# Kernel tuning notes

Hardware: AMD Instinct MI355X
Metric: run time of the kernel (lower is better)

Reference implementation:

```python
import jax, jax.numpy as jnp
import numpy as np

DIM = 256


def setup_inputs() -> dict:
    key = jax.random.key(0)
    ks = jax.random.split(key, 10)
    d = DIM
    inp = {
        "agent": jax.random.normal(ks[0], (64, d), dtype=jnp.float32),
        "x": jax.random.normal(ks[1], (8, 4096, d), dtype=jnp.float32),
        # parameters (stored as [in, out]; y = x @ W + b)
        "W_qkv": jax.random.normal(ks[2], (d, 3 * d), dtype=jnp.float32) * (d ** -0.5),
        "b_qkv": jnp.zeros((3 * d,), dtype=jnp.float32),
        "W_agent": jax.random.normal(ks[3], (d, 2 * d), dtype=jnp.float32) * (d ** -0.5),
        "b_agent": jnp.zeros((2 * d,), dtype=jnp.float32),
        "W_fc1": jax.random.normal(ks[4], (d, d), dtype=jnp.float32) * (d ** -0.5),
        "b_fc1": jnp.zeros((d,), dtype=jnp.float32),
        "W_fc2": jax.random.normal(ks[5], (d, d), dtype=jnp.float32) * (d ** -0.5),
        "b_fc2": jnp.zeros((d,), dtype=jnp.float32),
    }
    return inp


def reference(agent, x, W_qkv, b_qkv, W_agent, b_agent, W_fc1, b_fc1, W_fc2, b_fc2):
    d = x.shape[-1]
    scale = d ** -0.5
    # qkv projection of tokens: [B,N,3d] -> q,k,v each [B,N,d]
    qkv = x @ W_qkv + b_qkv
    q, k, v = jnp.split(qkv, 3, axis=-1)
    # agent projection: [K,2d] -> q_agent,k_agent each [K,d]
    ag = agent @ W_agent + b_agent
    q_agent, k_agent = jnp.split(ag, 2, axis=-1)
    # stage 1: agents attend over tokens -> [B,K,N]
    attn1 = jax.nn.softmax(jnp.einsum('kd,bnd->bkn', q_agent, k) * scale, axis=-1)
    va = jnp.einsum('bkn,bnd->bkd', attn1, v)  # [B,K,d]
    va = va @ W_fc1 + b_fc1
    # stage 2: tokens attend over agents -> [B,N,K]
    attn2 = jax.nn.softmax(jnp.einsum('bnd,kd->bnk', q, k_agent) * scale, axis=-1)
    out = jnp.einsum('bnk,bkd->bnd', attn2, va)  # [B,N,d]
    out = out @ W_fc2 + b_fc2
    return out + x
```

## Files before the change

kernel.cpp:

```cpp
#include <hip/hip_runtime.h>
#include <stdint.h>
#include <string.h>

#define BB 8
#define NN 4096
#define DD 256
#define SCALE 0.0625f
#define XS 264
#define XT 72

using frag_ab = __attribute__((ext_vector_type(8))) short;
using frag_cd = __attribute__((ext_vector_type(4))) float;

__device__ __forceinline__ unsigned short f2bf(float f) {
    union { float f; unsigned u; } a; a.f = f;
    unsigned r = a.u + 0x7FFFu + ((a.u >> 16) & 1u);
    return (unsigned short)(r >> 16);
}
__device__ __forceinline__ float bf2f(unsigned short h) {
    union { unsigned u; float f; } a; a.u = ((unsigned)h) << 16;
    return a.f;
}
__device__ __forceinline__ int xsw(int tok, int d) {
    const int e = ((tok >> 3) & 3) << 1;
    return tok * XS + (d & 7) + (((d >> 3) ^ e) << 3);
}

__global__ __launch_bounds__(256) void k_setup(
    const float* __restrict__ agent, const float* __restrict__ Wag,
    const float* __restrict__ bag, const float* __restrict__ Wqkv,
    const float* __restrict__ bqkv, const float* __restrict__ Wfc1,
    const float* __restrict__ bfc1, const float* __restrict__ Wfc2,
    unsigned short* __restrict__ P12t, float* __restrict__ c2,
    unsigned short* __restrict__ W3b, float* __restrict__ b3)
{
    __shared__ float arow[256];
    __shared__ float red[4][256];
    float* redf = &red[0][0];
    const int bx = blockIdx.x, tid = threadIdx.x;
    const int w = tid >> 6, lane = tid & 63;
    if (bx < 128) {
        const int c = bx;
        const int woff = (c < 64) ? 256 : 0;
        const int aoff = (c < 64) ? 0 : 256;
        const int row = c & 63;
        {
            float p4[4] = {0.f, 0.f, 0.f, 0.f};
            for (int oo = 0; oo < 64; ++oo) {
                const int o = w * 64 + oo;
                const float ao = agent[row * 256 + o];
#pragma unroll
                for (int jj = 0; jj < 4; ++jj)
                    p4[jj] += ao * Wag[o * 512 + aoff + jj * 64 + lane];
            }
#pragma unroll
            for (int jj = 0; jj < 4; ++jj) red[w][jj * 64 + lane] = p4[jj];
        }
        __syncthreads();
        arow[tid] = bag[aoff + tid] + red[0][tid] + red[1][tid] + red[2][tid] + red[3][tid];
        __syncthreads();
        {
            const float4* wr = (const float4*)&Wqkv[(size_t)tid * 768 + woff];
            float s = 0.f;
#pragma unroll 4
            for (int o4 = 0; o4 < 64; ++o4) {
                float4 v = wr[o4];
                s += v.x * arow[o4 * 4] + v.y * arow[o4 * 4 + 1] +
                     v.z * arow[o4 * 4 + 2] + v.w * arow[o4 * 4 + 3];
            }
            P12t[(size_t)c * 256 + tid] = f2bf(SCALE * s);
        }
        if (c >= 64) {
            __syncthreads();
            redf[tid] = bqkv[woff + tid] * arow[tid];
            __syncthreads();
            for (int st = 128; st; st >>= 1) {
                if (tid < st) redf[tid] += redf[tid + st];
                __syncthreads();
            }
            if (tid == 0) c2[c - 64] = SCALE * redf[0];
        }
    } else {
        const int i = bx - 128;
        const bool isb3 = (bx == 384);
        {
            float p4[4] = {0.f, 0.f, 0.f, 0.f};
            for (int oo = 0; oo < 64; ++oo) {
                const int o = w * 64 + oo;
                const float wv = isb3 ? bqkv[512 + o] : Wqkv[(size_t)i * 768 + 512 + o];
#pragma unroll
                for (int jj = 0; jj < 4; ++jj)
                    p4[jj] += wv * Wfc1[o * 256 + jj * 64 + lane];
            }
#pragma unroll
            for (int jj = 0; jj < 4; ++jj) red[w][jj * 64 + lane] = p4[jj];
        }
        __syncthreads();
        arow[tid] = (isb3 ? bfc1[tid] : 0.f) +
                    red[0][tid] + red[1][tid] + red[2][tid] + red[3][tid];
        __syncthreads();
        {
            float p4[4] = {0.f, 0.f, 0.f, 0.f};
            for (int kk = 0; kk < 64; ++kk) {
                const int k = w * 64 + kk;
                const float av = arow[k];
#pragma unroll
                for (int jj = 0; jj < 4; ++jj)
                    p4[jj] += av * Wfc2[k * 256 + jj * 64 + lane];
            }
#pragma unroll
            for (int jj = 0; jj < 4; ++jj) red[w][jj * 64 + lane] = p4[jj];
        }
        __syncthreads();
        const float o4 = red[0][tid] + red[1][tid] + red[2][tid] + red[3][tid];
        if (isb3) b3[tid] = o4;
        else      W3b[(size_t)i * 256 + tid] = f2bf(o4);
    }
}

__global__ __launch_bounds__(256) void k_fuse(
    const float* __restrict__ x, const unsigned short* __restrict__ P12t,
    const float* __restrict__ c2, unsigned short* __restrict__ p2b,
    unsigned short* __restrict__ part, float* __restrict__ statS)
{
    __shared__ unsigned short xtile[64 * XS];
    __shared__ unsigned short Pl[64 * XT];
    __shared__ float Ss[4][64];
    const int s = blockIdx.x, b = blockIdx.y;
    const int n0 = s * 64;
    const int tid = threadIdx.x;
    const int w = tid >> 6, lane = tid & 63;
    const int ml = lane & 15, q = lane >> 4;

#pragma unroll
    for (int p = 0; p < 16; ++p) {
        int idx = p * 256 + tid;
        int tok = idx >> 6, d = (idx & 63) * 4;
        float4 v = *(const float4*)&x[(size_t)(b * 4096 + n0 + tok) * 256 + d];
        unsigned short u[4] = {f2bf(v.x), f2bf(v.y), f2bf(v.z), f2bf(v.w)};
        uint2 pk; memcpy(&pk, u, 8);
        *(uint2*)&xtile[xsw(tok, d)] = pk;
    }
    __syncthreads();

    frag_ab afr[8];
#pragma unroll
    for (int kb4 = 0; kb4 < 4; ++kb4)
#pragma unroll
        for (int ks = 0; ks < 2; ++ks)
            afr[kb4 * 2 + ks] =
                *(const frag_ab*)&xtile[xsw(w * 16 + ml, kb4 * 64 + ks * 32 + q * 8)];

    frag_cd acc1[8];
#pragma unroll
    for (int j = 0; j < 8; ++j)
#pragma unroll
        for (int r = 0; r < 4; ++r) acc1[j][r] = 0.f;

    for (int kb4 = 0; kb4 < 4; ++kb4) {
#pragma unroll
        for (int ks = 0; ks < 2; ++ks) {
            const int kk = kb4 * 64 + ks * 32 + q * 8;
            const frag_ab a = afr[kb4 * 2 + ks];
#pragma unroll
            for (int j = 0; j < 8; ++j) {
                frag_ab bf = *(const frag_ab*)&P12t[(size_t)(j * 16 + ml) * 256 + kk];
                acc1[j] = __builtin_amdgcn_mfma_f32_16x16x32_bf16(a, bf, acc1[j], 0, 0, 0);
            }
        }
    }

    {
        float cc[4];
#pragma unroll
        for (int j = 0; j < 4; ++j) cc[j] = c2[j * 16 + ml];
#pragma unroll
        for (int r = 0; r < 4; ++r) {
            float e[4], sum = 0.f;
#pragma unroll
            for (int j = 0; j < 4; ++j) {
                e[j] = __expf(acc1[4 + j][r] + cc[j]);
                sum += e[j];
            }
#pragma unroll
            for (int mask = 1; mask <= 8; mask <<= 1) sum += __shfl_xor(sum, mask);
            float inv = 1.f / sum;
            const int tok = n0 + w * 16 + q * 4 + r;
#pragma unroll
            for (int j = 0; j < 4; ++j)
                p2b[(size_t)(b * 4096 + tok) * 64 + j * 16 + ml] = f2bf(e[j] * inv);
        }
    }

    float e1[4][4];
#pragma unroll
    for (int j = 0; j < 4; ++j) {
#pragma unroll
        for (int r = 0; r < 4; ++r) e1[j][r] = __expf(acc1[j][r]);
        float sj = e1[j][0] + e1[j][1] + e1[j][2] + e1[j][3];
        sj += __shfl_xor(sj, 16);
        sj += __shfl_xor(sj, 32);
        if (lane < 16) Ss[w][j * 16 + ml] = sj;
    }

#pragma unroll
    for (int j = 0; j < 4; ++j)
#pragma unroll
        for (int r = 0; r < 4; ++r)
            Pl[(j * 16 + ml) * XT + w * 16 + q * 4 + r] = f2bf(e1[j][r]);
    __syncthreads();

    if (tid < 64)
        statS[(size_t)(b * 64 + tid) * 64 + s] =
            Ss[0][tid] + Ss[1][tid] + Ss[2][tid] + Ss[3][tid];

    frag_cd acc2[4][4];
#pragma unroll
    for (int af = 0; af < 4; ++af)
#pragma unroll
        for (int i = 0; i < 4; ++i)
#pragma unroll
            for (int r = 0; r < 4; ++r) acc2[af][i][r] = 0.f;
#pragma unroll
    for (int ks = 0; ks < 2; ++ks) {
        const int kk = ks * 32 + q * 8;
        frag_ab a[4], bf[4];
#pragma unroll
        for (int af = 0; af < 4; ++af)
            a[af] = *(const frag_ab*)&Pl[(af * 16 + ml) * XT + kk];
#pragma unroll
        for (int i = 0; i < 4; ++i) {
            const int d = w * 64 + i * 16 + ml;
            unsigned short u[8];
#pragma unroll
            for (int t = 0; t < 8; ++t) u[t] = xtile[xsw(kk + t, d)];
            memcpy(&bf[i], u, 16);
        }
#pragma unroll
        for (int af = 0; af < 4; ++af)
#pragma unroll
            for (int i = 0; i < 4; ++i)
                acc2[af][i] = __builtin_amdgcn_mfma_f32_16x16x32_bf16(
                    a[af], bf[i], acc2[af][i], 0, 0, 0);
    }
#pragma unroll
    for (int af = 0; af < 4; ++af)
#pragma unroll
        for (int i = 0; i < 4; ++i)
#pragma unroll
            for (int r = 0; r < 4; ++r)
                part[(size_t)((s * 8 + b) * 64 + af * 16 + q * 4 + r) * 256 +
                     w * 64 + i * 16 + ml] = f2bf(acc2[af][i][r]);
}

__global__ __launch_bounds__(256) void k_fc(
    const unsigned short* __restrict__ part, const float* __restrict__ statS,
    const unsigned short* __restrict__ W3b, const float* __restrict__ b3,
    unsigned short* __restrict__ va3t)
{
    __shared__ float red[4][256];
    __shared__ float rowb[256];
    __shared__ float rs[64];
    const int row = blockIdx.x, tid = threadIdx.x;
    const int b = row >> 6, agc = row & 63;
    const int w = tid >> 6, lane = tid & 63;
    {
        float p4[4] = {0.f, 0.f, 0.f, 0.f};
        for (int ss = 0; ss < 16; ++ss) {
            const int s = w * 16 + ss;
            uint2 pk = *(const uint2*)&part[(size_t)((s * 8 + b) * 64 + agc) * 256 + lane * 4];
            unsigned short u[4]; memcpy(u, &pk, 8);
#pragma unroll
            for (int k = 0; k < 4; ++k) p4[k] += bf2f(u[k]);
        }
#pragma unroll
        for (int k = 0; k < 4; ++k) red[w][lane * 4 + k] = p4[k];
    }
    if (tid < 64) rs[tid] = statS[(size_t)(b * 64 + agc) * 64 + tid];
    __syncthreads();
    float tot = 0.f;
#pragma unroll
    for (int t = 0; t < 64; ++t) tot += rs[t];
    rowb[tid] = (red[0][tid] + red[1][tid] + red[2][tid] + red[3][tid]) / tot;
    __syncthreads();
    {
        float p4[4] = {0.f, 0.f, 0.f, 0.f};
        for (int kk = 0; kk < 64; ++kk) {
            const int k = w * 64 + kk;
            const float rv = rowb[k];
#pragma unroll
            for (int jj = 0; jj < 4; ++jj)
                p4[jj] += rv * bf2f(W3b[(size_t)k * 256 + jj * 64 + lane]);
        }
#pragma unroll
        for (int jj = 0; jj < 4; ++jj) red[w][jj * 64 + lane] = p4[jj];
    }
    __syncthreads();
    const float s2 = b3[tid] + red[0][tid] + red[1][tid] + red[2][tid] + red[3][tid];
    va3t[(size_t)(b * 256 + tid) * 64 + agc] = f2bf(s2);
}

__global__ __launch_bounds__(256) void k_stage2(
    const unsigned short* __restrict__ p2b, const unsigned short* __restrict__ va3t,
    const float* __restrict__ x, const float* __restrict__ bfc2,
    float* __restrict__ out)
{
    const int n0 = blockIdx.x * 32, b = blockIdx.y;
    const int tid = threadIdx.x;
    const int w = tid >> 6, lane = tid & 63;
    const int ml = lane & 15, q = lane >> 4;

    frag_cd acc[4][2];
#pragma unroll
    for (int i = 0; i < 4; ++i)
#pragma unroll
        for (int j = 0; j < 2; ++j)
#pragma unroll
            for (int r = 0; r < 4; ++r) acc[i][j][r] = 0.f;
#pragma unroll
    for (int ks = 0; ks < 2; ++ks) {
        const int kk = ks * 32 + q * 8;
        frag_ab a[4], bf[2];
#pragma unroll
        for (int i = 0; i < 4; ++i)
            a[i] = *(const frag_ab*)&va3t[(size_t)(b * 256 + w * 64 + i * 16 + ml) * 64 + kk];
#pragma unroll
        for (int j = 0; j < 2; ++j)
            bf[j] = *(const frag_ab*)&p2b[(size_t)(b * 4096 + n0 + j * 16 + ml) * 64 + kk];
#pragma unroll
        for (int i = 0; i < 4; ++i)
#pragma unroll
            for (int j = 0; j < 2; ++j)
                acc[i][j] = __builtin_amdgcn_mfma_f32_16x16x32_bf16(
                    a[i], bf[j], acc[i][j], 0, 0, 0);
    }

#pragma unroll
    for (int i = 0; i < 4; ++i) {
        const int d0 = w * 64 + i * 16 + q * 4;
        float4 bias = *(const float4*)&bfc2[d0];
#pragma unroll
        for (int j = 0; j < 2; ++j) {
            const int tok = n0 + j * 16 + ml;
            size_t ad = (size_t)(b * 4096 + tok) * 256 + d0;
            float4 xr = *(const float4*)&x[ad];
            float4 o;
            o.x = acc[i][j][0] + bias.x + xr.x;
            o.y = acc[i][j][1] + bias.y + xr.y;
            o.z = acc[i][j][2] + bias.z + xr.z;
            o.w = acc[i][j][3] + bias.w + xr.w;
            *(float4*)&out[ad] = o;
        }
    }
}

extern "C" void kernel_launch(void* const* d_in, const int* in_sizes, int n_in,
                              void* d_out, int out_size, void* d_ws, size_t ws_size,
                              hipStream_t stream) {
    const float* agent = (const float*)d_in[0];
    const float* x     = (const float*)d_in[1];
    const float* Wqkv  = (const float*)d_in[2];
    const float* bqkv  = (const float*)d_in[3];
    const float* Wag   = (const float*)d_in[4];
    const float* bag   = (const float*)d_in[5];
    const float* Wfc1  = (const float*)d_in[6];
    const float* bfc1  = (const float*)d_in[7];
    const float* Wfc2  = (const float*)d_in[8];
    const float* bfc2  = (const float*)d_in[9];
    float* out = (float*)d_out;

    char* wsp = (char*)d_ws;
    size_t off = 0;
    unsigned short* p2b  = (unsigned short*)(wsp + off); off += (size_t)BB * NN * 64 * 2;
    unsigned short* part = (unsigned short*)(wsp + off); off += (size_t)64 * BB * 64 * 256 * 2;
    float* statS = (float*)(wsp + off); off += (size_t)BB * 64 * 64 * 4;
    unsigned short* P12t = (unsigned short*)(wsp + off); off += (size_t)128 * 256 * 2;
    float* c2   = (float*)(wsp + off); off += 256 * 4;
    unsigned short* W3b = (unsigned short*)(wsp + off); off += (size_t)256 * 256 * 2;
    float* b3   = (float*)(wsp + off); off += 256 * 4;
    unsigned short* va3t = (unsigned short*)(wsp + off); off += (size_t)BB * DD * 64 * 2;

    k_setup<<<385, 256, 0, stream>>>(agent, Wag, bag, Wqkv, bqkv, Wfc1, bfc1, Wfc2,
                                     P12t, c2, W3b, b3);
    k_fuse<<<dim3(64, BB), 256, 0, stream>>>(x, P12t, c2, p2b, part, statS);
    k_fc<<<512, 256, 0, stream>>>(part, statS, W3b, b3, va3t);
    k_stage2<<<dim3(128, BB), 256, 0, stream>>>(p2b, va3t, x, bfc2, out);
}
```

Measured before the change: 164.5 us.

## Split k_fuse work across 8 waves and vectorize small-GEMM weight loads

k_fuse now launches 512 threads per block. Waves are split so half compute the stage-1 agent scores and the other half compute the stage-2 softmax columns, and the P·x product is split across 8 waves by agent-row block and half of d. This raises parallelism and cuts per-wave accumulator registers in the main fused kernel, which only has 512 blocks. Separately, the weight reads in the setup and fc kernels become per-lane float4/uint2 loads over contiguous columns, changing how the per-wave reduction buffer is indexed. The larger block can lower occupancy per CU, and each wave still loads its A fragments for the full K range.

```diff
diff --git a/kernel.cpp b/kernel.cpp
--- a/kernel.cpp
+++ b/kernel.cpp
@@ -39,6 +39,7 @@
     float* redf = &red[0][0];
     const int bx = blockIdx.x, tid = threadIdx.x;
     const int w = tid >> 6, lane = tid & 63;
+    const int c4 = lane * 4;
     if (bx < 128) {
         const int c = bx;
         const int woff = (c < 64) ? 256 : 0;
@@ -49,12 +50,12 @@
             for (int oo = 0; oo < 64; ++oo) {
                 const int o = w * 64 + oo;
                 const float ao = agent[row * 256 + o];
-#pragma unroll
-                for (int jj = 0; jj < 4; ++jj)
-                    p4[jj] += ao * Wag[o * 512 + aoff + jj * 64 + lane];
-            }
-#pragma unroll
-            for (int jj = 0; jj < 4; ++jj) red[w][jj * 64 + lane] = p4[jj];
+                float4 wv = *(const float4*)&Wag[o * 512 + aoff + c4];
+                p4[0] += ao * wv.x; p4[1] += ao * wv.y;
+                p4[2] += ao * wv.z; p4[3] += ao * wv.w;
+            }
+#pragma unroll
+            for (int jj = 0; jj < 4; ++jj) red[w][c4 + jj] = p4[jj];
         }
         __syncthreads();
         arow[tid] = bag[aoff + tid] + red[0][tid] + red[1][tid] + red[2][tid] + red[3][tid];
@@ -88,12 +89,12 @@
             for (int oo = 0; oo < 64; ++oo) {
                 const int o = w * 64 + oo;
                 const float wv = isb3 ? bqkv[512 + o] : Wqkv[(size_t)i * 768 + 512 + o];
-#pragma unroll
-                for (int jj = 0; jj < 4; ++jj)
-                    p4[jj] += wv * Wfc1[o * 256 + jj * 64 + lane];
-            }
-#pragma unroll
-            for (int jj = 0; jj < 4; ++jj) red[w][jj * 64 + lane] = p4[jj];
+                float4 f1 = *(const float4*)&Wfc1[o * 256 + c4];
+                p4[0] += wv * f1.x; p4[1] += wv * f1.y;
+                p4[2] += wv * f1.z; p4[3] += wv * f1.w;
+            }
+#pragma unroll
+            for (int jj = 0; jj < 4; ++jj) red[w][c4 + jj] = p4[jj];
         }
         __syncthreads();
         arow[tid] = (isb3 ? bfc1[tid] : 0.f) +
@@ -104,12 +105,12 @@
             for (int kk = 0; kk < 64; ++kk) {
                 const int k = w * 64 + kk;
                 const float av = arow[k];
-#pragma unroll
-                for (int jj = 0; jj < 4; ++jj)
-                    p4[jj] += av * Wfc2[k * 256 + jj * 64 + lane];
-            }
-#pragma unroll
-            for (int jj = 0; jj < 4; ++jj) red[w][jj * 64 + lane] = p4[jj];
+                float4 f2 = *(const float4*)&Wfc2[k * 256 + c4];
+                p4[0] += av * f2.x; p4[1] += av * f2.y;
+                p4[2] += av * f2.z; p4[3] += av * f2.w;
+            }
+#pragma unroll
+            for (int jj = 0; jj < 4; ++jj) red[w][c4 + jj] = p4[jj];
         }
         __syncthreads();
         const float o4 = red[0][tid] + red[1][tid] + red[2][tid] + red[3][tid];
@@ -118,7 +119,7 @@
     }
 }
 
-__global__ __launch_bounds__(256) void k_fuse(
+__global__ __launch_bounds__(512) void k_fuse(
     const float* __restrict__ x, const unsigned short* __restrict__ P12t,
     const float* __restrict__ c2, unsigned short* __restrict__ p2b,
     unsigned short* __restrict__ part, float* __restrict__ statS)
@@ -131,10 +132,11 @@
     const int tid = threadIdx.x;
     const int w = tid >> 6, lane = tid & 63;
     const int ml = lane & 15, q = lane >> 4;
-
-#pragma unroll
-    for (int p = 0; p < 16; ++p) {
-        int idx = p * 256 + tid;
+    const int rt = w & 3, cg = w >> 2;
+
+#pragma unroll
+    for (int p = 0; p < 8; ++p) {
+        int idx = p * 512 + tid;
         int tok = idx >> 6, d = (idx & 63) * 4;
         float4 v = *(const float4*)&x[(size_t)(b * 4096 + n0 + tok) * 256 + d];
         unsigned short u[4] = {f2bf(v.x), f2bf(v.y), f2bf(v.z), f2bf(v.w)};
@@ -149,11 +151,11 @@
 #pragma unroll
         for (int ks = 0; ks < 2; ++ks)
             afr[kb4 * 2 + ks] =
-                *(const frag_ab*)&xtile[xsw(w * 16 + ml, kb4 * 64 + ks * 32 + q * 8)];
-
-    frag_cd acc1[8];
-#pragma unroll
-    for (int j = 0; j < 8; ++j)
+                *(const frag_ab*)&xtile[xsw(rt * 16 + ml, kb4 * 64 + ks * 32 + q * 8)];
+
+    frag_cd acc1[4];
+#pragma unroll
+    for (int j = 0; j < 4; ++j)
 #pragma unroll
         for (int r = 0; r < 4; ++r) acc1[j][r] = 0.f;
 
@@ -163,14 +165,15 @@
             const int kk = kb4 * 64 + ks * 32 + q * 8;
             const frag_ab a = afr[kb4 * 2 + ks];
 #pragma unroll
-            for (int j = 0; j < 8; ++j) {
-                frag_ab bf = *(const frag_ab*)&P12t[(size_t)(j * 16 + ml) * 256 + kk];
+            for (int j = 0; j < 4; ++j) {
+                frag_ab bf = *(const frag_ab*)
+                    &P12t[(size_t)(cg * 64 + j * 16 + ml) * 256 + kk];
                 acc1[j] = __builtin_amdgcn_mfma_f32_16x16x32_bf16(a, bf, acc1[j], 0, 0, 0);
             }
         }
     }
 
-    {
+    if (cg == 1) {
         float cc[4];
 #pragma unroll
         for (int j = 0; j < 4; ++j) cc[j] = c2[j * 16 + ml];
@@ -179,78 +182,68 @@
             float e[4], sum = 0.f;
 #pragma unroll
             for (int j = 0; j < 4; ++j) {
-                e[j] = __expf(acc1[4 + j][r] + cc[j]);
+                e[j] = __expf(acc1[j][r] + cc[j]);
                 sum += e[j];
             }
 #pragma unroll
             for (int mask = 1; mask <= 8; mask <<= 1) sum += __shfl_xor(sum, mask);
             float inv = 1.f / sum;
-            const int tok = n0 + w * 16 + q * 4 + r;
+            const int tok = n0 + rt * 16 + q * 4 + r;
 #pragma unroll
             for (int j = 0; j < 4; ++j)
                 p2b[(size_t)(b * 4096 + tok) * 64 + j * 16 + ml] = f2bf(e[j] * inv);
         }
-    }
-
-    float e1[4][4];
-#pragma unroll
-    for (int j = 0; j < 4; ++j) {
-#pragma unroll
-        for (int r = 0; r < 4; ++r) e1[j][r] = __expf(acc1[j][r]);
-        float sj = e1[j][0] + e1[j][1] + e1[j][2] + e1[j][3];
-        sj += __shfl_xor(sj, 16);
-        sj += __shfl_xor(sj, 32);
-        if (lane < 16) Ss[w][j * 16 + ml] = sj;
-    }
-
-#pragma unroll
-    for (int j = 0; j < 4; ++j)
-#pragma unroll
-        for (int r = 0; r < 4; ++r)
-            Pl[(j * 16 + ml) * XT + w * 16 + q * 4 + r] = f2bf(e1[j][r]);
+    } else {
+        float e1[4][4];
+#pragma unroll
+        for (int j = 0; j < 4; ++j) {
+#pragma unroll
+            for (int r = 0; r < 4; ++r) e1[j][r] = __expf(acc1[j][r]);
+            float sj = e1[j][0] + e1[j][1] + e1[j][2] + e1[j][3];
+            sj += __shfl_xor(sj, 16);
+            sj += __shfl_xor(sj, 32);
+            if (lane < 16) Ss[rt][j * 16 + ml] = sj;
+        }
+#pragma unroll
+        for (int j = 0; j < 4; ++j)
+#pragma unroll
+            for (int r = 0; r < 4; ++r)
+                Pl[(j * 16 + ml) * XT + rt * 16 + q * 4 + r] = f2bf(e1[j][r]);
+    }
     __syncthreads();
 
     if (tid < 64)
         statS[(size_t)(b * 64 + tid) * 64 + s] =
             Ss[0][tid] + Ss[1][tid] + Ss[2][tid] + Ss[3][tid];
 
-    frag_cd acc2[4][4];
-#pragma unroll
-    for (int af = 0; af < 4; ++af)
-#pragma unroll
-        for (int i = 0; i < 4; ++i)
-#pragma unroll
-            for (int r = 0; r < 4; ++r) acc2[af][i][r] = 0.f;
-#pragma unroll
-    for (int ks = 0; ks < 2; ++ks) {
-        const int kk = ks * 32 + q * 8;
-        frag_ab a[4], bf[4];
-#pragma unroll
-        for (int af = 0; af < 4; ++af)
-            a[af] = *(const frag_ab*)&Pl[(af * 16 + ml) * XT + kk];
-#pragma unroll
-        for (int i = 0; i < 4; ++i) {
-            const int d = w * 64 + i * 16 + ml;
-            unsigned short u[8];
-#pragma unroll
-            for (int t = 0; t < 8; ++t) u[t] = xtile[xsw(kk + t, d)];
-            memcpy(&bf[i], u, 16);
-        }
-#pragma unroll
-        for (int af = 0; af < 4; ++af)
-#pragma unroll
-            for (int i = 0; i < 4; ++i)
-                acc2[af][i] = __builtin_amdgcn_mfma_f32_16x16x32_bf16(
-                    a[af], bf[i], acc2[af][i], 0, 0, 0);
-    }
-#pragma unroll
-    for (int af = 0; af < 4; ++af)
-#pragma unroll
-        for (int i = 0; i < 4; ++i)
+    {
+        const int af = w & 3, dh = w >> 2;
+        frag_cd acc2[8];
+#pragma unroll
+        for (int i = 0; i < 8; ++i)
+#pragma unroll
+            for (int r = 0; r < 4; ++r) acc2[i][r] = 0.f;
+#pragma unroll
+        for (int ks = 0; ks < 2; ++ks) {
+            const int kk = ks * 32 + q * 8;
+            frag_ab a = *(const frag_ab*)&Pl[(af * 16 + ml) * XT + kk];
+#pragma unroll
+            for (int i = 0; i < 8; ++i) {
+                const int d = dh * 128 + i * 16 + ml;
+                unsigned short u[8];
+#pragma unroll
+                for (int t = 0; t < 8; ++t) u[t] = xtile[xsw(kk + t, d)];
+                frag_ab bf; memcpy(&bf, u, 16);
+                acc2[i] = __builtin_amdgcn_mfma_f32_16x16x32_bf16(a, bf, acc2[i], 0, 0, 0);
+            }
+        }
+#pragma unroll
+        for (int i = 0; i < 8; ++i)
 #pragma unroll
             for (int r = 0; r < 4; ++r)
                 part[(size_t)((s * 8 + b) * 64 + af * 16 + q * 4 + r) * 256 +
-                     w * 64 + i * 16 + ml] = f2bf(acc2[af][i][r]);
+                     dh * 128 + i * 16 + ml] = f2bf(acc2[i][r]);
+    }
 }
 
 __global__ __launch_bounds__(256) void k_fc(
@@ -264,17 +257,18 @@
     const int row = blockIdx.x, tid = threadIdx.x;
     const int b = row >> 6, agc = row & 63;
     const int w = tid >> 6, lane = tid & 63;
+    const int c4 = lane * 4;
     {
         float p4[4] = {0.f, 0.f, 0.f, 0.f};
         for (int ss = 0; ss < 16; ++ss) {
             const int s = w * 16 + ss;
-            uint2 pk = *(const uint2*)&part[(size_t)((s * 8 + b) * 64 + agc) * 256 + lane * 4];
+            uint2 pk = *(const uint2*)&part[(size_t)((s * 8 + b) * 64 + agc) * 256 + c4];
             unsigned short u[4]; memcpy(u, &pk, 8);
 #pragma unroll
             for (int k = 0; k < 4; ++k) p4[k] += bf2f(u[k]);
         }
 #pragma unroll
-        for (int k = 0; k < 4; ++k) red[w][lane * 4 + k] = p4[k];
+        for (int k = 0; k < 4; ++k) red[w][c4 + k] = p4[k];
     }
     if (tid < 64) rs[tid] = statS[(size_t)(b * 64 + agc) * 64 + tid];
     __syncthreads();
@@ -288,12 +282,13 @@
         for (int kk = 0; kk < 64; ++kk) {
             const int k = w * 64 + kk;
             const float rv = rowb[k];
-#pragma unroll
-            for (int jj = 0; jj < 4; ++jj)
-                p4[jj] += rv * bf2f(W3b[(size_t)k * 256 + jj * 64 + lane]);
-        }
-#pragma unroll
-        for (int jj = 0; jj < 4; ++jj) red[w][jj * 64 + lane] = p4[jj];
+            uint2 pk = *(const uint2*)&W3b[(size_t)k * 256 + c4];
+            unsigned short u[4]; memcpy(u, &pk, 8);
+#pragma unroll
+            for (int jj = 0; jj < 4; ++jj) p4[jj] += rv * bf2f(u[jj]);
+        }
+#pragma unroll
+        for (int jj = 0; jj < 4; ++jj) red[w][c4 + jj] = p4[jj];
     }
     __syncthreads();
     const float s2 = b3[tid] + red[0][tid] + red[1][tid] + red[2][tid] + red[3][tid];
@@ -382,7 +377,7 @@
 
     k_setup<<<385, 256, 0, stream>>>(agent, Wag, bag, Wqkv, bqkv, Wfc1, bfc1, Wfc2,
                                      P12t, c2, W3b, b3);
-    k_fuse<<<dim3(64, BB), 256, 0, stream>>>(x, P12t, c2, p2b, part, statS);
+    k_fuse<<<dim3(64, BB), 512, 0, stream>>>(x, P12t, c2, p2b, part, statS);
     k_fc<<<512, 256, 0, stream>>>(part, statS, W3b, b3, va3t);
     k_stage2<<<dim3(128, BB), 256, 0, stream>>>(p2b, va3t, x, bfc2, out);
 }
```

Measured after the change: 173.6 us. 1.05x slower.

## Drop LDS x tile in k_fuse and vectorize weight loads in setup/fc

Applied to the files above, without the earlier changes.

k_fuse no longer stages the 64-token x tile into swizzled shared memory. MFMA A fragments are now built straight from global float4 loads, and the stage-1 B fragments come from strided scalar global loads (8 tokens apart, 256 floats each), converted to bf16 on the fly. This removes the tile's LDS footprint and the barrier, which may allow more resident blocks, but x is read from global twice and the transposed reads are uncoalesced. Separately, k_setup and k_fc switch per-lane weight reads to float4/uint2 vector loads, with each lane owning four contiguous output columns.

```diff
diff --git a/kernel.cpp b/kernel.cpp
--- a/kernel.cpp
+++ b/kernel.cpp
@@ -6,7 +6,6 @@
 #define NN 4096
 #define DD 256
 #define SCALE 0.0625f
-#define XS 264
 #define XT 72
 
 using frag_ab = __attribute__((ext_vector_type(8))) short;
@@ -20,10 +19,6 @@
 __device__ __forceinline__ float bf2f(unsigned short h) {
     union { unsigned u; float f; } a; a.u = ((unsigned)h) << 16;
     return a.f;
-}
-__device__ __forceinline__ int xsw(int tok, int d) {
-    const int e = ((tok >> 3) & 3) << 1;
-    return tok * XS + (d & 7) + (((d >> 3) ^ e) << 3);
 }
 
 __global__ __launch_bounds__(256) void k_setup(
@@ -39,6 +34,7 @@
     float* redf = &red[0][0];
     const int bx = blockIdx.x, tid = threadIdx.x;
     const int w = tid >> 6, lane = tid & 63;
+    const int c4 = lane * 4;
     if (bx < 128) {
         const int c = bx;
         const int woff = (c < 64) ? 256 : 0;
@@ -49,12 +45,12 @@
             for (int oo = 0; oo < 64; ++oo) {
                 const int o = w * 64 + oo;
                 const float ao = agent[row * 256 + o];
-#pragma unroll
-                for (int jj = 0; jj < 4; ++jj)
-                    p4[jj] += ao * Wag[o * 512 + aoff + jj * 64 + lane];
-            }
-#pragma unroll
-            for (int jj = 0; jj < 4; ++jj) red[w][jj * 64 + lane] = p4[jj];
+                float4 wv = *(const float4*)&Wag[o * 512 + aoff + c4];
+                p4[0] += ao * wv.x; p4[1] += ao * wv.y;
+                p4[2] += ao * wv.z; p4[3] += ao * wv.w;
+            }
+#pragma unroll
+            for (int jj = 0; jj < 4; ++jj) red[w][c4 + jj] = p4[jj];
         }
         __syncthreads();
         arow[tid] = bag[aoff + tid] + red[0][tid] + red[1][tid] + red[2][tid] + red[3][tid];
@@ -88,12 +84,12 @@
             for (int oo = 0; oo < 64; ++oo) {
                 const int o = w * 64 + oo;
                 const float wv = isb3 ? bqkv[512 + o] : Wqkv[(size_t)i * 768 + 512 + o];
-#pragma unroll
-                for (int jj = 0; jj < 4; ++jj)
-                    p4[jj] += wv * Wfc1[o * 256 + jj * 64 + lane];
-            }
-#pragma unroll
-            for (int jj = 0; jj < 4; ++jj) red[w][jj * 64 + lane] = p4[jj];
+                float4 f1 = *(const float4*)&Wfc1[o * 256 + c4];
+                p4[0] += wv * f1.x; p4[1] += wv * f1.y;
+                p4[2] += wv * f1.z; p4[3] += wv * f1.w;
+            }
+#pragma unroll
+            for (int jj = 0; jj < 4; ++jj) red[w][c4 + jj] = p4[jj];
         }
         __syncthreads();
         arow[tid] = (isb3 ? bfc1[tid] : 0.f) +
@@ -104,12 +100,12 @@
             for (int kk = 0; kk < 64; ++kk) {
                 const int k = w * 64 + kk;
                 const float av = arow[k];
-#pragma unroll
-                for (int jj = 0; jj < 4; ++jj)
-                    p4[jj] += av * Wfc2[k * 256 + jj * 64 + lane];
-            }
-#pragma unroll
-            for (int jj = 0; jj < 4; ++jj) red[w][jj * 64 + lane] = p4[jj];
+                float4 f2 = *(const float4*)&Wfc2[k * 256 + c4];
+                p4[0] += av * f2.x; p4[1] += av * f2.y;
+                p4[2] += av * f2.z; p4[3] += av * f2.w;
+            }
+#pragma unroll
+            for (int jj = 0; jj < 4; ++jj) red[w][c4 + jj] = p4[jj];
         }
         __syncthreads();
         const float o4 = red[0][tid] + red[1][tid] + red[2][tid] + red[3][tid];
@@ -123,7 +119,6 @@
     const float* __restrict__ c2, unsigned short* __restrict__ p2b,
     unsigned short* __restrict__ part, float* __restrict__ statS)
 {
-    __shared__ unsigned short xtile[64 * XS];
     __shared__ unsigned short Pl[64 * XT];
     __shared__ float Ss[4][64];
     const int s = blockIdx.x, b = blockIdx.y;
@@ -132,36 +127,22 @@
     const int w = tid >> 6, lane = tid & 63;
     const int ml = lane & 15, q = lane >> 4;
 
-#pragma unroll
-    for (int p = 0; p < 16; ++p) {
-        int idx = p * 256 + tid;
-        int tok = idx >> 6, d = (idx & 63) * 4;
-        float4 v = *(const float4*)&x[(size_t)(b * 4096 + n0 + tok) * 256 + d];
-        unsigned short u[4] = {f2bf(v.x), f2bf(v.y), f2bf(v.z), f2bf(v.w)};
-        uint2 pk; memcpy(&pk, u, 8);
-        *(uint2*)&xtile[xsw(tok, d)] = pk;
-    }
-    __syncthreads();
-
-    frag_ab afr[8];
-#pragma unroll
-    for (int kb4 = 0; kb4 < 4; ++kb4)
-#pragma unroll
-        for (int ks = 0; ks < 2; ++ks)
-            afr[kb4 * 2 + ks] =
-                *(const frag_ab*)&xtile[xsw(w * 16 + ml, kb4 * 64 + ks * 32 + q * 8)];
-
+    const float* xrow = &x[(size_t)(b * 4096 + n0 + w * 16 + ml) * 256];
     frag_cd acc1[8];
 #pragma unroll
     for (int j = 0; j < 8; ++j)
 #pragma unroll
         for (int r = 0; r < 4; ++r) acc1[j][r] = 0.f;
 
-    for (int kb4 = 0; kb4 < 4; ++kb4) {
+    for (int kb = 0; kb < 4; ++kb) {
 #pragma unroll
         for (int ks = 0; ks < 2; ++ks) {
-            const int kk = kb4 * 64 + ks * 32 + q * 8;
-            const frag_ab a = afr[kb4 * 2 + ks];
+            const int kk = kb * 64 + ks * 32 + q * 8;
+            float4 lo = *(const float4*)&xrow[kk];
+            float4 hi = *(const float4*)&xrow[kk + 4];
+            unsigned short u[8] = {f2bf(lo.x), f2bf(lo.y), f2bf(lo.z), f2bf(lo.w),
+                                   f2bf(hi.x), f2bf(hi.y), f2bf(hi.z), f2bf(hi.w)};
+            frag_ab a; memcpy(&a, u, 16);
 #pragma unroll
             for (int j = 0; j < 8; ++j) {
                 frag_ab bf = *(const frag_ab*)&P12t[(size_t)(j * 16 + ml) * 256 + kk];
@@ -231,9 +212,10 @@
 #pragma unroll
         for (int i = 0; i < 4; ++i) {
             const int d = w * 64 + i * 16 + ml;
+            const float* xc = &x[(size_t)(b * 4096 + n0 + kk) * 256 + d];
             unsigned short u[8];
 #pragma unroll
-            for (int t = 0; t < 8; ++t) u[t] = xtile[xsw(kk + t, d)];
+            for (int t = 0; t < 8; ++t) u[t] = f2bf(xc[(size_t)t * 256]);
             memcpy(&bf[i], u, 16);
         }
 #pragma unroll
@@ -264,17 +246,18 @@
     const int row = blockIdx.x, tid = threadIdx.x;
     const int b = row >> 6, agc = row & 63;
     const int w = tid >> 6, lane = tid & 63;
+    const int c4 = lane * 4;
     {
         float p4[4] = {0.f, 0.f, 0.f, 0.f};
         for (int ss = 0; ss < 16; ++ss) {
             const int s = w * 16 + ss;
-            uint2 pk = *(const uint2*)&part[(size_t)((s * 8 + b) * 64 + agc) * 256 + lane * 4];
+            uint2 pk = *(const uint2*)&part[(size_t)((s * 8 + b) * 64 + agc) * 256 + c4];
             unsigned short u[4]; memcpy(u, &pk, 8);
 #pragma unroll
             for (int k = 0; k < 4; ++k) p4[k] += bf2f(u[k]);
         }
 #pragma unroll
-        for (int k = 0; k < 4; ++k) red[w][lane * 4 + k] = p4[k];
+        for (int k = 0; k < 4; ++k) red[w][c4 + k] = p4[k];
     }
     if (tid < 64) rs[tid] = statS[(size_t)(b * 64 + agc) * 64 + tid];
     __syncthreads();
@@ -288,12 +271,13 @@
         for (int kk = 0; kk < 64; ++kk) {
             const int k = w * 64 + kk;
             const float rv = rowb[k];
-#pragma unroll
-            for (int jj = 0; jj < 4; ++jj)
-                p4[jj] += rv * bf2f(W3b[(size_t)k * 256 + jj * 64 + lane]);
-        }
-#pragma unroll
-        for (int jj = 0; jj < 4; ++jj) red[w][jj * 64 + lane] = p4[jj];
+            uint2 pk = *(const uint2*)&W3b[(size_t)k * 256 + c4];
+            unsigned short u[4]; memcpy(u, &pk, 8);
+#pragma unroll
+            for (int jj = 0; jj < 4; ++jj) p4[jj] += rv * bf2f(u[jj]);
+        }
+#pragma unroll
+        for (int jj = 0; jj < 4; ++jj) red[w][c4 + jj] = p4[jj];
     }
     __syncthreads();
     const float s2 = b3[tid] + red[0][tid] + red[1][tid] + red[2][tid] + red[3][tid];
```

Measured after the change: 184.0 us. +11.8%, slower.
